# Optimization experiments

Hardware: AMD Instinct MI355X
Metric: run time of the kernel (lower is better)

The kernel has to match this reference:

```python
import jax, jax.numpy as jnp
import numpy as np
from jax import lax

WINDOW_SIZE = 11
SIGMA = 1.5
DATA_RANGE = 1.0
EPS = 1e-8


def _gauss_1d(window_size=WINDOW_SIZE, sigma=SIGMA):
    coords = jnp.arange(window_size, dtype=jnp.float32) - window_size // 2
    g = jnp.exp(-(coords ** 2) / (2.0 * sigma ** 2))
    return g / g.sum()


def _gaussian_filter(x, w1d):
    # Separable depthwise blur: horizontal then vertical, VALID padding (use_padding=False).
    C = x.shape[1]
    win = w1d.shape[0]
    kh = jnp.broadcast_to(w1d.reshape(1, 1, 1, win), (C, 1, 1, win))  # OIHW, groups=C
    kv = jnp.broadcast_to(w1d.reshape(1, 1, win, 1), (C, 1, win, 1))
    dn = ('NCHW', 'OIHW', 'NCHW')
    out = lax.conv_general_dilated(x, kh, (1, 1), 'VALID',
                                   dimension_numbers=dn, feature_group_count=C)
    out = lax.conv_general_dilated(out, kv, (1, 1), 'VALID',
                                   dimension_numbers=dn, feature_group_count=C)
    return out


def setup_inputs() -> dict:
    key = jax.random.key(0)
    k1, k2 = jax.random.split(key)
    B, C, H, W = 16, 3, 768, 768
    X = jax.random.uniform(k1, (B, C, H, W), dtype=jnp.float32)
    Y = jax.random.uniform(k2, (B, C, H, W), dtype=jnp.float32)
    window = _gauss_1d()
    return {"X": X, "Y": Y, "window": window}


def reference(X, Y, window):
    K1, K2 = 0.01, 0.03
    C1 = (K1 * DATA_RANGE) ** 2
    C2 = (K2 * DATA_RANGE) ** 2
    mu_x = _gaussian_filter(X, window)
    mu_y = _gaussian_filter(Y, window)
    sigma_x = _gaussian_filter(X * X, window) - mu_x ** 2
    sigma_y = _gaussian_filter(Y * Y, window) - mu_y ** 2
    sigma_xy = _gaussian_filter(X * Y, window) - mu_x * mu_y
    cs = (2.0 * sigma_xy + C2) / (sigma_x + sigma_y + C2 + EPS)
    cs = jax.nn.relu(cs)
    ssim_map = (2.0 * mu_x * mu_y + C1) / (mu_x ** 2 + mu_y ** 2 + C1 + EPS) * cs
    ssim_val = ssim_map.mean(axis=(1, 2, 3))  # [B]
    return ssim_val
```

## Files before the change

kernel.cpp:

```cpp
#include <hip/hip_runtime.h>


typedef float f32x2 __attribute__((ext_vector_type(2)));

#define H_IMG 768
#define W_IMG 768
#define OH 758
#define OW_TOT 758
#define OWS 256
#define NSEG 16

static __device__ __forceinline__ f32x2 mk2(float a, float b) {
    f32x2 r; r.x = a; r.y = b; return r;
}

__global__ void ssim_zero_out(float* __restrict__ out) {
    if (threadIdx.x < 16) out[threadIdx.x] = 0.0f;
}

__attribute__((amdgpu_flat_work_group_size(256, 256), amdgpu_waves_per_eu(3, 3)))
__global__ void ssim_fused(const float* __restrict__ X, const float* __restrict__ Y,
                           const float* __restrict__ Wg, float* __restrict__ out) {
    const float C1 = 1e-4f, C2 = 9e-4f, EPS = 1e-8f;
    const float INV_COUNT = 1.0f / (3.0f * 758.0f * 758.0f);

    const int t = threadIdx.x;
    int bx = blockIdx.x;
    const int seg = bx & (NSEG - 1); bx >>= 4;
    const int strip = bx % 3; bx /= 3;
    const int ch = bx % 3;
    const int b  = bx / 3;

    const int R0 = (OH * seg) / NSEG;
    const int Rend = (OH * (seg + 1)) / NSEG;
    const int hseg = Rend - R0;
    const int c0 = strip * OWS;

    const float* Xi = X + (size_t)(b * 3 + ch) * (H_IMG * W_IMG);
    const float* Yi = Y + (size_t)(b * 3 + ch) * (H_IMG * W_IMG);

    f32x2 ww[11];
#pragma unroll
    for (int k = 0; k < 11; ++k) { float wk = Wg[k]; ww[k] = mk2(wk, wk); }

    __shared__ float hb[4][4][OWS];
    __shared__ float red[4];

    const int sA = t >> 6;
    const int cg = t & 63;
    const int colbase = c0 + 4 * cg;
    const int k0 = min(colbase,      W_IMG - 4);
    const int k1 = min(colbase + 4,  W_IMG - 4);
    const int k2 = min(colbase + 8,  W_IMG - 4);
    const int k3 = min(colbase + 12, W_IMG - 2);

    f32x2 rg01[16], rg23[16];
#pragma unroll
    for (int j = 0; j < 16; ++j) { rg01[j] = mk2(0.f, 0.f); rg23[j] = mk2(0.f, 0.f); }

    const bool colok = (c0 + t) < OW_TOT;
    float local = 0.0f;
    const int M = (hseg + 13) >> 2;

    for (int mb = 0; mb < M; mb += 4) {
#pragma unroll
        for (int p = 0; p < 4; ++p) {
            const int m = mb + p;
            if (m < M) {
                {
                    int r = R0 + 4 * m + sA;
                    r = min(r, H_IMG - 1);
                    const float* xr = Xi + (size_t)r * W_IMG;
                    const float* yr = Yi + (size_t)r * W_IMG;
                    float4 xa = *(const float4*)(xr + k0);
                    float4 xb = *(const float4*)(xr + k1);
                    float4 xc = *(const float4*)(xr + k2);
                    float2 xd = *(const float2*)(xr + k3);
                    float4 ya = *(const float4*)(yr + k0);
                    float4 yb = *(const float4*)(yr + k1);
                    float4 yc = *(const float4*)(yr + k2);
                    float2 yd = *(const float2*)(yr + k3);
                    f32x2 v[14] = {
                        mk2(xa.x, ya.x), mk2(xa.y, ya.y), mk2(xa.z, ya.z), mk2(xa.w, ya.w),
                        mk2(xb.x, yb.x), mk2(xb.y, yb.y), mk2(xb.z, yb.z), mk2(xb.w, yb.w),
                        mk2(xc.x, yc.x), mk2(xc.y, yc.y), mk2(xc.z, yc.z), mk2(xc.w, yc.w),
                        mk2(xd.x, yd.x), mk2(xd.y, yd.y)};

                    {
                        f32x2 hm[4];
#pragma unroll
                        for (int cc = 0; cc < 4; ++cc) {
                            f32x2 a = mk2(0.f, 0.f);
#pragma unroll
                            for (int k = 0; k < 11; ++k)
                                a = __builtin_elementwise_fma(ww[k], v[cc + k], a);
                            hm[cc] = a;
                        }
                        *(float4*)&hb[sA][0][4 * cg] = make_float4(hm[0].x, hm[1].x, hm[2].x, hm[3].x);
                        *(float4*)&hb[sA][1][4 * cg] = make_float4(hm[0].y, hm[1].y, hm[2].y, hm[3].y);
                    }
#pragma unroll
                    for (int j = 0; j < 14; ++j) {
                        const float xx = v[j].x, yy = v[j].y;
                        v[j] = mk2(fmaf(xx, xx, yy * yy), xx * yy);
                    }
                    {
                        f32x2 hs[4];
#pragma unroll
                        for (int cc = 0; cc < 4; ++cc) {
                            f32x2 a = mk2(0.f, 0.f);
#pragma unroll
                            for (int k = 0; k < 11; ++k)
                                a = __builtin_elementwise_fma(ww[k], v[cc + k], a);
                            hs[cc] = a;
                        }
                        *(float4*)&hb[sA][2][4 * cg] = make_float4(hs[0].x, hs[1].x, hs[2].x, hs[3].x);
                        *(float4*)&hb[sA][3][4 * cg] = make_float4(hs[0].y, hs[1].y, hs[2].y, hs[3].y);
                    }
                }
                __syncthreads();

                {
#pragma unroll
                    for (int s2 = 0; s2 < 4; ++s2) {
                        const int sl = (4 * p + s2) & 15;
                        rg01[sl] = mk2(hb[s2][0][t], hb[s2][1][t]);
                        rg23[sl] = mk2(hb[s2][2][t], hb[s2][3][t]);
                    }
#pragma unroll
                    for (int s2 = 0; s2 < 4; ++s2) {
                        const int orel = 4 * m - 10 + s2;
                        f32x2 a01 = mk2(0.f, 0.f), a23 = mk2(0.f, 0.f);
#pragma unroll
                        for (int k = 0; k < 11; ++k) {
                            const int sl = (4 * p + s2 + k + 6) & 15;
                            a01 = __builtin_elementwise_fma(ww[k], rg01[sl], a01);
                            a23 = __builtin_elementwise_fma(ww[k], rg23[sl], a23);
                        }
                        const float a0 = a01.x, a1 = a01.y, a2 = a23.x, a3 = a23.y;
                        const float mux2 = a0 * a0;
                        const float muy2 = a1 * a1;
                        const float mxy  = a0 * a1;
                        const float sigsum = a2 - mux2 - muy2;
                        const float sxy    = a3 - mxy;
                        const float num = (2.0f * mxy + C1) * (2.0f * sxy + C2);
                        const float den = (mux2 + muy2 + C1 + EPS) * (sigsum + C2 + EPS);
                        const float v = fmaxf(__fdividef(num, den), 0.0f);
                        if (colok && (orel >= 0) && (orel < hseg)) local += v;
                    }
                }
                __syncthreads();
            }
        }
    }

    float v = local;
#pragma unroll
    for (int off = 32; off > 0; off >>= 1) v += __shfl_down(v, off, 64);
    if ((t & 63) == 0) red[t >> 6] = v;
    __syncthreads();
    if (t == 0) {
        atomicAdd(&out[b], (red[0] + red[1] + red[2] + red[3]) * INV_COUNT);
    }
}

extern "C" void kernel_launch(void* const* d_in, const int* in_sizes, int n_in,
                              void* d_out, int out_size, void* d_ws, size_t ws_size,
                              hipStream_t stream) {
    const float* X  = (const float*)d_in[0];
    const float* Y  = (const float*)d_in[1];
    const float* Wg = (const float*)d_in[2];
    float* out = (float*)d_out;

    hipLaunchKernelGGL(ssim_zero_out, dim3(1), dim3(64), 0, stream, out);
    hipLaunchKernelGGL(ssim_fused, dim3(16 * 3 * 3 * NSEG), dim3(256), 0, stream,
                       X, Y, Wg, out);
}
```

Measured before the change: 282.8 us.

## Prefetch next row block into registers and double-buffer shared memory

Loads the next block of X/Y rows into a second register set while the current block is being filtered, so global loads overlap with compute. The shared horizontal-blur buffer is double-buffered by iteration parity, which removes the second __syncthreads per iteration. This roughly doubles register usage for the raw row data and doubles shared memory, which may hurt occupancy under the fixed waves-per-EU hint. With a single barrier, a write to buffer pb two iterations later is ordered after the reads of pb by the intervening barrier.

```diff
diff --git a/kernel.cpp b/kernel.cpp
--- a/kernel.cpp
+++ b/kernel.cpp
@@ -14,6 +14,24 @@
     f32x2 r; r.x = a; r.y = b; return r;
 }
 
+struct RowRegs {
+    float4 xa, xb, xc, ya, yb, yc;
+    float2 xd, yd;
+};
+
+static __device__ __forceinline__ void load_rows(RowRegs& rr,
+        const float* __restrict__ xr, const float* __restrict__ yr,
+        int k0, int k1, int k2, int k3) {
+    rr.xa = *(const float4*)(xr + k0);
+    rr.xb = *(const float4*)(xr + k1);
+    rr.xc = *(const float4*)(xr + k2);
+    rr.xd = *(const float2*)(xr + k3);
+    rr.ya = *(const float4*)(yr + k0);
+    rr.yb = *(const float4*)(yr + k1);
+    rr.yc = *(const float4*)(yr + k2);
+    rr.yd = *(const float2*)(yr + k3);
+}
+
 __global__ void ssim_zero_out(float* __restrict__ out) {
     if (threadIdx.x < 16) out[threadIdx.x] = 0.0f;
 }
@@ -43,7 +61,7 @@
 #pragma unroll
     for (int k = 0; k < 11; ++k) { float wk = Wg[k]; ww[k] = mk2(wk, wk); }
 
-    __shared__ float hb[4][4][OWS];
+    __shared__ float hb[2][4][4][OWS];
     __shared__ float red[4];
 
     const int sA = t >> 6;
@@ -62,29 +80,37 @@
     float local = 0.0f;
     const int M = (hseg + 13) >> 2;
 
+    RowRegs r0, r1;
+    {
+        int rr = min(R0 + sA, H_IMG - 1);
+        load_rows(r0, Xi + (size_t)rr * W_IMG, Yi + (size_t)rr * W_IMG, k0, k1, k2, k3);
+    }
+
     for (int mb = 0; mb < M; mb += 4) {
 #pragma unroll
         for (int p = 0; p < 4; ++p) {
             const int m = mb + p;
             if (m < M) {
+                const int pb = p & 1;
+                RowRegs& cur = pb ? r1 : r0;
+                RowRegs& nxt = pb ? r0 : r1;
+
+                if (m + 1 < M) {
+                    int rn = R0 + 4 * (m + 1) + sA;
+                    rn = min(rn, H_IMG - 1);
+                    load_rows(nxt, Xi + (size_t)rn * W_IMG, Yi + (size_t)rn * W_IMG,
+                              k0, k1, k2, k3);
+                }
+
                 {
-                    int r = R0 + 4 * m + sA;
-                    r = min(r, H_IMG - 1);
-                    const float* xr = Xi + (size_t)r * W_IMG;
-                    const float* yr = Yi + (size_t)r * W_IMG;
-                    float4 xa = *(const float4*)(xr + k0);
-                    float4 xb = *(const float4*)(xr + k1);
-                    float4 xc = *(const float4*)(xr + k2);
-                    float2 xd = *(const float2*)(xr + k3);
-                    float4 ya = *(const float4*)(yr + k0);
-                    float4 yb = *(const float4*)(yr + k1);
-                    float4 yc = *(const float4*)(yr + k2);
-                    float2 yd = *(const float2*)(yr + k3);
                     f32x2 v[14] = {
-                        mk2(xa.x, ya.x), mk2(xa.y, ya.y), mk2(xa.z, ya.z), mk2(xa.w, ya.w),
-                        mk2(xb.x, yb.x), mk2(xb.y, yb.y), mk2(xb.z, yb.z), mk2(xb.w, yb.w),
-                        mk2(xc.x, yc.x), mk2(xc.y, yc.y), mk2(xc.z, yc.z), mk2(xc.w, yc.w),
-                        mk2(xd.x, yd.x), mk2(xd.y, yd.y)};
+                        mk2(cur.xa.x, cur.ya.x), mk2(cur.xa.y, cur.ya.y),
+                        mk2(cur.xa.z, cur.ya.z), mk2(cur.xa.w, cur.ya.w),
+                        mk2(cur.xb.x, cur.yb.x), mk2(cur.xb.y, cur.yb.y),
+                        mk2(cur.xb.z, cur.yb.z), mk2(cur.xb.w, cur.yb.w),
+                        mk2(cur.xc.x, cur.yc.x), mk2(cur.xc.y, cur.yc.y),
+                        mk2(cur.xc.z, cur.yc.z), mk2(cur.xc.w, cur.yc.w),
+                        mk2(cur.xd.x, cur.yd.x), mk2(cur.xd.y, cur.yd.y)};
 
                     {
                         f32x2 hm[4];
@@ -96,8 +122,8 @@
                                 a = __builtin_elementwise_fma(ww[k], v[cc + k], a);
                             hm[cc] = a;
                         }
-                        *(float4*)&hb[sA][0][4 * cg] = make_float4(hm[0].x, hm[1].x, hm[2].x, hm[3].x);
-                        *(float4*)&hb[sA][1][4 * cg] = make_float4(hm[0].y, hm[1].y, hm[2].y, hm[3].y);
+                        *(float4*)&hb[pb][sA][0][4 * cg] = make_float4(hm[0].x, hm[1].x, hm[2].x, hm[3].x);
+                        *(float4*)&hb[pb][sA][1][4 * cg] = make_float4(hm[0].y, hm[1].y, hm[2].y, hm[3].y);
                     }
 #pragma unroll
                     for (int j = 0; j < 14; ++j) {
@@ -114,8 +140,8 @@
                                 a = __builtin_elementwise_fma(ww[k], v[cc + k], a);
                             hs[cc] = a;
                         }
-                        *(float4*)&hb[sA][2][4 * cg] = make_float4(hs[0].x, hs[1].x, hs[2].x, hs[3].x);
-                        *(float4*)&hb[sA][3][4 * cg] = make_float4(hs[0].y, hs[1].y, hs[2].y, hs[3].y);
+                        *(float4*)&hb[pb][sA][2][4 * cg] = make_float4(hs[0].x, hs[1].x, hs[2].x, hs[3].x);
+                        *(float4*)&hb[pb][sA][3][4 * cg] = make_float4(hs[0].y, hs[1].y, hs[2].y, hs[3].y);
                     }
                 }
                 __syncthreads();
@@ -124,8 +150,8 @@
 #pragma unroll
                     for (int s2 = 0; s2 < 4; ++s2) {
                         const int sl = (4 * p + s2) & 15;
-                        rg01[sl] = mk2(hb[s2][0][t], hb[s2][1][t]);
-                        rg23[sl] = mk2(hb[s2][2][t], hb[s2][3][t]);
+                        rg01[sl] = mk2(hb[pb][s2][0][t], hb[pb][s2][1][t]);
+                        rg23[sl] = mk2(hb[pb][s2][2][t], hb[pb][s2][3][t]);
                     }
 #pragma unroll
                     for (int s2 = 0; s2 < 4; ++s2) {
@@ -149,7 +175,6 @@
                         if (colok && (orel >= 0) && (orel < hseg)) local += v;
                     }
                 }
-                __syncthreads();
             }
         }
     }
```

Result: faster. 275.0 us (-2.7%).
